# Kernel tuning notes

Measured on AMD Instinct MI355X. Metric: run time of the kernel, lower is better.

Reference implementation:

```python
import jax, jax.numpy as jnp
import numpy as np

DX = 1.0
DY = 1.0
W_DIV = 1e9
W_SMOOTH = 10.0
W_STD = 100.0
EPS = 1e-10


def _corner(a, i, j, k):
    # slice dims 2,3,4: 0 -> [0:-1], 1 -> [1:]
    sl = lambda b: slice(1, None) if b else slice(0, -1)
    return a[:, :, sl(i), sl(j), sl(k)]


def setup_inputs() -> dict:
    key = jax.random.key(0)
    k1, k2 = jax.random.split(key)
    outputs = jax.random.normal(k1, (2, 1, 256, 256, 64), dtype=jnp.float32)
    targets = jax.random.normal(k2, (2, 3, 256, 256, 64), dtype=jnp.float32)
    return {"outputs": outputs, "targets": targets}


def _loss(outputs, targets):
    bx, by, bz = targets[:, 0:1], targets[:, 1:2], targets[:, 2:3]
    z = outputs[:, 0:1]

    # vertical thickness and smoothness of its square
    dz = z[..., 1:] - z[..., :-1]
    dz2 = dz ** 2
    lap = (6 * dz2[:, :, 1:-1, 1:-1, 1:-1]
           - dz2[:, :, :-2, 1:-1, 1:-1] - dz2[:, :, 2:, 1:-1, 1:-1]
           - dz2[:, :, 1:-1, :-2, 1:-1] - dz2[:, :, 1:-1, 2:, 1:-1]
           - dz2[:, :, 1:-1, 1:-1, 2:] - dz2[:, :, 1:-1, 1:-1, :-2])
    loss_smooth = jnp.mean(lap ** 2)

    # per-(batch, channel, z) std over the spatial plane (unbiased, matching torch.std)
    loss_std = jnp.mean(jnp.std(dz, axis=(2, 3), ddof=1))

    # 8 cell corners for each field
    corners = lambda a: {(i, j, k): _corner(a, i, j, k)
                         for i in (0, 1) for j in (0, 1) for k in (0, 1)}
    BX, BY, BZ, Z = corners(bx), corners(by), corners(bz), corners(z)

    az = lambda a, b: jnp.abs(Z[a] - Z[b])
    num = (0.25 * (BX[1,0,0] + BX[1,1,0] + BX[1,0,1] + BX[1,1,1]) * DY * 0.5 * (az((1,0,1),(1,0,0)) + az((1,1,1),(1,1,0)))
           - 0.25 * (BX[0,0,0] + BX[0,1,0] + BX[0,0,1] + BX[0,1,1]) * DY * 0.5 * (az((0,0,1),(0,0,0)) + az((0,1,1),(0,1,0)))
           + 0.25 * (BY[0,1,0] + BY[1,1,0] + BY[0,1,1] + BY[1,1,1]) * DX * 0.5 * (az((0,1,1),(0,1,0)) + az((1,1,1),(1,1,0)))
           - 0.25 * (BY[0,0,0] + BY[1,0,0] + BY[0,0,1] + BY[1,0,1]) * DX * 0.5 * (az((0,0,1),(0,0,0)) + az((1,0,1),(1,0,0)))
           + 0.25 * (BZ[0,0,1] + BZ[0,1,1] + BZ[1,0,1] + BZ[1,1,1]) * DX * DY
           - 0.25 * (BZ[0,0,0] + BZ[0,1,0] + BZ[1,0,0] + BZ[1,1,0]) * DX * DY
           + (BX[0,0,1] + BX[1,0,1] + BX[1,1,1]) * DY * (Z[0,0,1] - Z[1,0,1]) / 6
           + (BX[0,1,1] + BX[1,1,1] + BX[1,0,1]) * DY * (Z[0,1,1] - Z[1,1,1]) / 6
           + (BY[1,0,1] + BY[1,1,1] + BY[0,1,1]) * DX * (Z[1,0,1] - Z[1,1,1]) / 6
           + (BY[0,0,1] + BY[0,1,1] + BY[1,1,1]) * DX * (Z[0,0,1] - Z[0,1,1]) / 6
           - (BX[0,0,0] + BX[1,0,0] + BX[1,1,0]) * DY * (Z[0,0,0] - Z[1,0,0]) / 6
           - (BX[0,1,0] + BX[1,1,0] + BX[1,0,0]) * DY * (Z[0,1,0] - Z[1,1,0]) / 6
           - (BY[1,0,0] + BY[1,1,0] + BY[0,1,0]) * DX * (Z[1,0,0] - Z[1,1,0]) / 6
           - (BY[0,0,0] + BY[0,1,0] + BY[1,1,0]) * DX * (Z[0,0,0] - Z[0,1,0]) / 6)

    sum8 = lambda C: sum(C.values())
    den = ((sum8(BX) * 0.125) ** 2 + (sum8(BY) * 0.125) ** 2
           + (sum8(BZ) * 0.125) ** 2 + EPS)
    loss_div = jnp.mean(num ** 2 / den)

    return loss_div * W_DIV, loss_smooth * W_SMOOTH + loss_std * W_STD


def reference(outputs, targets):
    return _loss(outputs, targets)
```

## Files before the change

### kernel.cpp

```cpp
#include <hip/hip_runtime.h>
#include <math.h>


#define ZSTR 388
#define BSTR 324
#define BFLD 1620

__global__ __launch_bounds__(512) void zero_ws_kernel(float* ws) {
    for (int i = threadIdx.x; i < 32 * 258; i += 512) ws[i] = 0.0f;
}

#define LD5(arr, p) do { \
    float4 _a = *(const float4*)(p); float4 _b = *(const float4*)((p) + 4); \
    arr[0] = _a.x; arr[1] = _a.y; arr[2] = _a.z; arr[3] = _a.w; arr[4] = _b.x; } while (0)

__global__ __launch_bounds__(256, 4) void fused_loss_kernel(
    const float* __restrict__ zin, const float* __restrict__ tg,
    float* __restrict__ ws)
{
    __shared__ float zs[6 * ZSTR];
    __shared__ float bs[3 * BFLD];
    __shared__ float rsc[4][2];

    const int tid  = threadIdx.x;
    const int lane = tid & 63;
    const int w    = tid >> 6;

    const int bb = blockIdx.x >> 12;
    const int rest = blockIdx.x & 4095;
    const int x0 = ((rest >> 6) & 63) << 2;
    const int y0 = (rest & 63) << 2;

    const float* zg = zin + ((size_t)bb << 22);

    for (int i = tid; i < 1776; i += 256) {
        if (i < 576) {
            int row = i >> 4;
            int o   = (i & 15) << 2;
            int xi  = row / 6;
            int yr  = row - xi * 6;
            int x = x0 - 1 + xi; x = x < 0 ? 0 : (x > 255 ? 255 : x);
            int y = y0 - 1 + yr; y = y < 0 ? 0 : (y > 255 ? 255 : y);
            *(float4*)&zs[xi * ZSTR + yr * 64 + o] =
                *(const float4*)&zg[x * 16384 + y * 64 + o];
        } else {
            int j  = i - 576;
            int f  = j / 400;
            int jj = j - f * 400;
            int row = jj >> 4;
            int o   = (jj & 15) << 2;
            int xi  = row / 5;
            int yr  = row - xi * 5;
            int x = x0 + xi; x = x > 255 ? 255 : x;
            int y = y0 + yr; y = y > 255 ? 255 : y;
            const float* g = tg + ((size_t)(bb * 3 + f) << 22);
            *(float4*)&bs[f * BFLD + xi * BSTR + yr * 64 + o] =
                *(const float4*)&g[x * 16384 + y * 64 + o];
        }
    }
    __syncthreads();

    const int c  = tid >> 4;
    const int kq = tid & 15;
    const int cx = c & 3, cy = c >> 2;
    const int xg = x0 + cx, yg = y0 + cy;
    const int k0 = kq << 2;

    const float* zC = &zs[(cx + 1) * ZSTR + (cy + 1) * 64 + k0];

    float zcv[7];
    {
        float4 m = *(const float4*)(zC - 4);
        float4 a = *(const float4*)(zC);
        float4 b = *(const float4*)(zC + 4);
        zcv[0] = m.w; zcv[1] = a.x; zcv[2] = a.y; zcv[3] = a.z; zcv[4] = a.w;
        zcv[5] = b.x; zcv[6] = b.y;
    }
    float zEv[5];  LD5(zEv,  zC + ZSTR);
    float zWv[5];  LD5(zWv,  zC - ZSTR);
    float zNv[5];  LD5(zNv,  zC + 64);
    float zSv[5];  LD5(zSv,  zC - 64);
    float zNEv[5]; LD5(zNEv, zC + ZSTR + 64);

    float dz0[4], dzE[4], dzN[4], dzNE[4];
    #pragma unroll
    for (int e = 0; e < 4; ++e) {
        dz0[e]  = zcv[e + 2] - zcv[e + 1];
        dzE[e]  = zEv[e + 1] - zEv[e];
        dzN[e]  = zNv[e + 1] - zNv[e];
        dzNE[e] = zNEv[e + 1] - zNEv[e];
    }

    float s1a[4], s2a[4];
    #pragma unroll
    for (int e = 0; e < 4; ++e) {
        bool kok = (k0 + e) < 63;
        s1a[e] = kok ? dz0[e] : 0.0f;
        s2a[e] = kok ? dz0[e] * dz0[e] : 0.0f;
    }

    float sm = 0.0f;
    if (xg >= 1 && xg <= 254 && yg >= 1 && yg <= 254) {
        #pragma unroll
        for (int e = 0; e < 4; ++e) {
            int k = k0 + e;
            if (k >= 1 && k <= 61) {
                float dzm = zcv[e + 1] - zcv[e];
                float dzp = zcv[e + 3] - zcv[e + 2];
                float dzw = zWv[e + 1] - zWv[e];
                float dzs = zSv[e + 1] - zSv[e];
                float lap = 6.0f * dz0[e] * dz0[e]
                          - dzw * dzw - dzE[e] * dzE[e]
                          - dzs * dzs - dzN[e] * dzN[e]
                          - dzm * dzm - dzp * dzp;
                sm += lap * lap;
            }
        }
    }

    float dv = 0.0f;
    if (xg < 255 && yg < 255) {
        const float* bxP = &bs[cx * BSTR + cy * 64 + k0];
        const float* byP = bxP + BFLD;
        const float* bzP = byP + BFLD;
        float bx00v[5]; LD5(bx00v, bxP);
        float bx10v[5]; LD5(bx10v, bxP + BSTR);
        float bx01v[5]; LD5(bx01v, bxP + 64);
        float bx11v[5]; LD5(bx11v, bxP + BSTR + 64);
        float by00v[5]; LD5(by00v, byP);
        float by10v[5]; LD5(by10v, byP + BSTR);
        float by01v[5]; LD5(by01v, byP + 64);
        float by11v[5]; LD5(by11v, byP + BSTR + 64);
        float bz00v[5]; LD5(bz00v, bzP);
        float bz10v[5]; LD5(bz10v, bzP + BSTR);
        float bz01v[5]; LD5(bz01v, bzP + 64);
        float bz11v[5]; LD5(bz11v, bzP + BSTR + 64);

        const float c6 = 1.0f / 6.0f;
        #pragma unroll
        for (int e = 0; e < 4; ++e) {
            if ((k0 + e) < 63) {
                float adz00 = fabsf(dz0[e]),  adz10 = fabsf(dzE[e]);
                float adz01 = fabsf(dzN[e]),  adz11 = fabsf(dzNE[e]);

                float num =
                    0.125f * ( (bx10v[e] + bx10v[e+1] + bx11v[e] + bx11v[e+1]) * (adz10 + adz11)
                             - (bx00v[e] + bx00v[e+1] + bx01v[e] + bx01v[e+1]) * (adz00 + adz01)
                             + (by01v[e] + by01v[e+1] + by11v[e] + by11v[e+1]) * (adz01 + adz11)
                             - (by00v[e] + by00v[e+1] + by10v[e] + by10v[e+1]) * (adz00 + adz10) )
                  + 0.25f * ( (bz00v[e+1] + bz10v[e+1] + bz01v[e+1] + bz11v[e+1])
                            - (bz00v[e]   + bz10v[e]   + bz01v[e]   + bz11v[e]) );

                num += c6 * ( (bx00v[e+1] + bx10v[e+1] + bx11v[e+1]) * (zcv[e+2] - zEv[e+1])
                            + (bx01v[e+1] + bx11v[e+1] + bx10v[e+1]) * (zNv[e+1] - zNEv[e+1])
                            + (by10v[e+1] + by11v[e+1] + by01v[e+1]) * (zEv[e+1] - zNEv[e+1])
                            + (by00v[e+1] + by01v[e+1] + by11v[e+1]) * (zcv[e+2] - zNv[e+1])
                            - (bx00v[e] + bx10v[e] + bx11v[e]) * (zcv[e+1] - zEv[e])
                            - (bx01v[e] + bx11v[e] + bx10v[e]) * (zNv[e] - zNEv[e])
                            - (by10v[e] + by11v[e] + by01v[e]) * (zEv[e] - zNEv[e])
                            - (by00v[e] + by01v[e] + by11v[e]) * (zcv[e+1] - zNv[e]) );

                float sbx = bx00v[e] + bx00v[e+1] + bx10v[e] + bx10v[e+1]
                          + bx01v[e] + bx01v[e+1] + bx11v[e] + bx11v[e+1];
                float sby = by00v[e] + by00v[e+1] + by10v[e] + by10v[e+1]
                          + by01v[e] + by01v[e+1] + by11v[e] + by11v[e+1];
                float sbz = bz00v[e] + bz00v[e+1] + bz10v[e] + bz10v[e+1]
                          + bz01v[e] + bz01v[e+1] + bz11v[e] + bz11v[e+1];
                float den = 0.015625f * (sbx * sbx + sby * sby + sbz * sbz) + 1e-10f;
                dv += num * num / den;
            }
        }
    }

    #pragma unroll
    for (int off = 32; off > 0; off >>= 1) {
        sm += __shfl_down(sm, off, 64);
        dv += __shfl_down(dv, off, 64);
    }

    __syncthreads();
    float* r1 = zs;
    float* r2 = zs + 1024;
    { float4 v; v.x = s1a[0]; v.y = s1a[1]; v.z = s1a[2]; v.w = s1a[3];
      *(float4*)&r1[tid << 2] = v; }
    { float4 v; v.x = s2a[0]; v.y = s2a[1]; v.z = s2a[2]; v.w = s2a[3];
      *(float4*)&r2[tid << 2] = v; }
    if (lane == 0) { rsc[w][0] = sm; rsc[w][1] = dv; }
    __syncthreads();

    if (tid < 64) {
        float a = 0.0f, b2 = 0.0f;
        #pragma unroll
        for (int cc = 0; cc < 16; ++cc) {
            a  += r1[cc * 64 + tid];
            b2 += r2[cc * 64 + tid];
        }
        float* sl = ws + (blockIdx.x & 31) * 258;
        if (tid < 63) {
            atomicAdd(&sl[2 + bb * 64 + tid],   a);
            atomicAdd(&sl[130 + bb * 64 + tid], b2);
        }
        if (tid == 0) atomicAdd(&sl[0], rsc[0][0] + rsc[1][0] + rsc[2][0] + rsc[3][0]);
        if (tid == 1) atomicAdd(&sl[1], rsc[0][1] + rsc[1][1] + rsc[2][1] + rsc[3][1]);
    }
}

__global__ __launch_bounds__(128) void finalize_kernel(const float* __restrict__ ws,
                                                       float* __restrict__ out)
{
    __shared__ double red[128];
    const int t = threadIdx.x;
    double stdv = 0.0;
    {
        int k = t & 63, bb = t >> 6;
        if (k < 63) {
            double s1 = 0.0, s2 = 0.0;
            for (int p = 0; p < 32; ++p) {
                s1 += (double)ws[p * 258 + 2 + bb * 64 + k];
                s2 += (double)ws[p * 258 + 130 + bb * 64 + k];
            }
            const double N = 65536.0;
            double var = (s2 - s1 * s1 / N) / (N - 1.0);
            stdv = sqrt(var > 0.0 ? var : 0.0);
        }
    }
    red[t] = stdv;
    __syncthreads();
    for (int off = 64; off > 0; off >>= 1) {
        if (t < off) red[t] += red[t + off];
        __syncthreads();
    }
    if (t == 0) {
        double smt = 0.0, dvt = 0.0;
        for (int p = 0; p < 32; ++p) {
            smt += (double)ws[p * 258 + 0];
            dvt += (double)ws[p * 258 + 1];
        }
        double loss_std    = red[0] / 126.0;
        double loss_smooth = smt / (2.0 * 254.0 * 254.0 * 61.0);
        double loss_div    = dvt / (2.0 * 255.0 * 255.0 * 63.0);
        out[0] = (float)(loss_div * 1e9);
        out[1] = (float)(loss_smooth * 10.0 + loss_std * 100.0);
    }
}

extern "C" void kernel_launch(void* const* d_in, const int* in_sizes, int n_in,
                              void* d_out, int out_size, void* d_ws, size_t ws_size,
                              hipStream_t stream) {
    const float* z  = (const float*)d_in[0];
    const float* tg = (const float*)d_in[1];
    float* out = (float*)d_out;
    float* ws  = (float*)d_ws;

    zero_ws_kernel<<<1, 512, 0, stream>>>(ws);
    fused_loss_kernel<<<8192, 256, 0, stream>>>(z, tg, ws);
    finalize_kernel<<<1, 128, 0, stream>>>(ws, out);
}
```

Before: 206.9 us.

## Load target field corners directly from global memory instead of staging in LDS

Drops the shared-memory staging buffer for the three target fields. Each thread now reads its 12 corner vectors straight from global memory, issued before the z-stencil work so their latency can overlap it, and clamps coordinates at the edges. Occupancy hint raised from 4 to 5 blocks per CU because LDS use falls. The trade-off is redundant global/L2 traffic, since neighbouring threads reread overlapping corners, plus more live registers holding the loaded values.

Measured after the change: 433.5 us. 2.1x slower.

```diff
diff --git a/kernel.cpp b/kernel.cpp
--- a/kernel.cpp
+++ b/kernel.cpp
@@ -3,8 +3,6 @@
 
 
 #define ZSTR 388
-#define BSTR 324
-#define BFLD 1620
 
 __global__ __launch_bounds__(512) void zero_ws_kernel(float* ws) {
     for (int i = threadIdx.x; i < 32 * 258; i += 512) ws[i] = 0.0f;
@@ -14,12 +12,16 @@
     float4 _a = *(const float4*)(p); float4 _b = *(const float4*)((p) + 4); \
     arr[0] = _a.x; arr[1] = _a.y; arr[2] = _a.z; arr[3] = _a.w; arr[4] = _b.x; } while (0)
 
-__global__ __launch_bounds__(256, 4) void fused_loss_kernel(
+#define LDG5(arr, p) do { \
+    float4 _a = *(const float4*)(p); \
+    arr[0] = _a.x; arr[1] = _a.y; arr[2] = _a.z; arr[3] = _a.w; \
+    arr[4] = (p)[t4]; } while (0)
+
+__global__ __launch_bounds__(256, 5) void fused_loss_kernel(
     const float* __restrict__ zin, const float* __restrict__ tg,
     float* __restrict__ ws)
 {
     __shared__ float zs[6 * ZSTR];
-    __shared__ float bs[3 * BFLD];
     __shared__ float rsc[4][2];
 
     const int tid  = threadIdx.x;
@@ -33,30 +35,15 @@
 
     const float* zg = zin + ((size_t)bb << 22);
 
-    for (int i = tid; i < 1776; i += 256) {
-        if (i < 576) {
-            int row = i >> 4;
-            int o   = (i & 15) << 2;
-            int xi  = row / 6;
-            int yr  = row - xi * 6;
-            int x = x0 - 1 + xi; x = x < 0 ? 0 : (x > 255 ? 255 : x);
-            int y = y0 - 1 + yr; y = y < 0 ? 0 : (y > 255 ? 255 : y);
-            *(float4*)&zs[xi * ZSTR + yr * 64 + o] =
-                *(const float4*)&zg[x * 16384 + y * 64 + o];
-        } else {
-            int j  = i - 576;
-            int f  = j / 400;
-            int jj = j - f * 400;
-            int row = jj >> 4;
-            int o   = (jj & 15) << 2;
-            int xi  = row / 5;
-            int yr  = row - xi * 5;
-            int x = x0 + xi; x = x > 255 ? 255 : x;
-            int y = y0 + yr; y = y > 255 ? 255 : y;
-            const float* g = tg + ((size_t)(bb * 3 + f) << 22);
-            *(float4*)&bs[f * BFLD + xi * BSTR + yr * 64 + o] =
-                *(const float4*)&g[x * 16384 + y * 64 + o];
-        }
+    for (int i = tid; i < 576; i += 256) {
+        int row = i >> 4;
+        int o   = (i & 15) << 2;
+        int xi  = row / 6;
+        int yr  = row - xi * 6;
+        int x = x0 - 1 + xi; x = x < 0 ? 0 : (x > 255 ? 255 : x);
+        int y = y0 - 1 + yr; y = y < 0 ? 0 : (y > 255 ? 255 : y);
+        *(float4*)&zs[xi * ZSTR + yr * 64 + o] =
+            *(const float4*)&zg[x * 16384 + y * 64 + o];
     }
     __syncthreads();
 
@@ -65,6 +52,27 @@
     const int cx = c & 3, cy = c >> 2;
     const int xg = x0 + cx, yg = y0 + cy;
     const int k0 = kq << 2;
+
+    const int xgc = xg > 254 ? 254 : xg;
+    const int ygc = yg > 254 ? 254 : yg;
+    const int t4  = (kq == 15) ? 0 : 4;
+    const float* b0 = tg + (((size_t)bb * 3) << 22)
+                         + (size_t)xgc * 16384 + (size_t)ygc * 64 + k0;
+    const float* b1 = b0 + 4194304;
+    const float* b2 = b0 + 8388608;
+
+    float bx00v[5]; LDG5(bx00v, b0);
+    float bx10v[5]; LDG5(bx10v, b0 + 16384);
+    float bx01v[5]; LDG5(bx01v, b0 + 64);
+    float bx11v[5]; LDG5(bx11v, b0 + 16448);
+    float by00v[5]; LDG5(by00v, b1);
+    float by10v[5]; LDG5(by10v, b1 + 16384);
+    float by01v[5]; LDG5(by01v, b1 + 64);
+    float by11v[5]; LDG5(by11v, b1 + 16448);
+    float bz00v[5]; LDG5(bz00v, b2);
+    float bz10v[5]; LDG5(bz10v, b2 + 16384);
+    float bz01v[5]; LDG5(bz01v, b2 + 64);
+    float bz11v[5]; LDG5(bz11v, b2 + 16448);
 
     const float* zC = &zs[(cx + 1) * ZSTR + (cy + 1) * 64 + k0];
 
@@ -120,22 +128,6 @@
 
     float dv = 0.0f;
     if (xg < 255 && yg < 255) {
-        const float* bxP = &bs[cx * BSTR + cy * 64 + k0];
-        const float* byP = bxP + BFLD;
-        const float* bzP = byP + BFLD;
-        float bx00v[5]; LD5(bx00v, bxP);
-        float bx10v[5]; LD5(bx10v, bxP + BSTR);
-        float bx01v[5]; LD5(bx01v, bxP + 64);
-        float bx11v[5]; LD5(bx11v, bxP + BSTR + 64);
-        float by00v[5]; LD5(by00v, byP);
-        float by10v[5]; LD5(by10v, byP + BSTR);
-        float by01v[5]; LD5(by01v, byP + 64);
-        float by11v[5]; LD5(by11v, byP + BSTR + 64);
-        float bz00v[5]; LD5(bz00v, bzP);
-        float bz10v[5]; LD5(bz10v, bzP + BSTR);
-        float bz01v[5]; LD5(bz01v, bzP + 64);
-        float bz11v[5]; LD5(bz11v, bzP + BSTR + 64);
-
         const float c6 = 1.0f / 6.0f;
         #pragma unroll
         for (int e = 0; e < 4; ++e) {
@@ -189,16 +181,16 @@
     __syncthreads();
 
     if (tid < 64) {
-        float a = 0.0f, b2 = 0.0f;
+        float a = 0.0f, b2r = 0.0f;
         #pragma unroll
         for (int cc = 0; cc < 16; ++cc) {
-            a  += r1[cc * 64 + tid];
-            b2 += r2[cc * 64 + tid];
+            a   += r1[cc * 64 + tid];
+            b2r += r2[cc * 64 + tid];
         }
         float* sl = ws + (blockIdx.x & 31) * 258;
         if (tid < 63) {
             atomicAdd(&sl[2 + bb * 64 + tid],   a);
-            atomicAdd(&sl[130 + bb * 64 + tid], b2);
+            atomicAdd(&sl[130 + bb * 64 + tid], b2r);
         }
         if (tid == 0) atomicAdd(&sl[0], rsc[0][0] + rsc[1][0] + rsc[2][0] + rsc[3][0]);
         if (tid == 1) atomicAdd(&sl[1], rsc[0][1] + rsc[1][1] + rsc[2][1] + rsc[3][1]);
```
